# Kernel tuning notes

Hardware: AMD Instinct MI355X
Metric: run time of the kernel (lower is better)

The kernel has to match this reference:

```python
import jax, jax.numpy as jnp
import numpy as np

NUM_HEADS = 8
SIZE_Q = 512
SIZE_K = 512
SIZE_V = 512
B, S = 2, 2048


def setup_inputs() -> dict:
    key = jax.random.key(0)
    ks = jax.random.split(key, 16)
    Hk = SIZE_K  # num_heads * head_size_k
    Hv = SIZE_V  # num_heads * head_size_v
    inp = {
        "k": jax.random.normal(ks[0], (B, S, SIZE_K), jnp.float32),
        "v": jax.random.normal(ks[1], (B, S, SIZE_V), jnp.float32),
        "q": jax.random.normal(ks[2], (B, S, SIZE_Q), jnp.float32),
        "mask": jax.random.randint(ks[3], (S, S), 0, 2).astype(jnp.bool_),
        "spatial_bias": jax.random.normal(ks[4], (1, NUM_HEADS, S, S), jnp.float32),
        # Linear params stored as [in, out]; y = x @ W + b
        "Wq": jax.random.normal(ks[5], (SIZE_Q, Hk), jnp.float32) / np.sqrt(SIZE_Q),
        "bq": jnp.zeros((Hk,), jnp.float32),
        "Wk": jax.random.normal(ks[6], (SIZE_K, Hk), jnp.float32) / np.sqrt(SIZE_K),
        "bk": jnp.zeros((Hk,), jnp.float32),
        "Wv": jax.random.normal(ks[7], (SIZE_V, Hv), jnp.float32) / np.sqrt(SIZE_V),
        "bv": jnp.zeros((Hv,), jnp.float32),
        "Wo": jax.random.normal(ks[8], (Hv, SIZE_V), jnp.float32) / np.sqrt(Hv),
        "bo": jnp.zeros((SIZE_V,), jnp.float32),
    }
    return inp


def reference(k, v, q, mask, spatial_bias, Wq, bq, Wk, bk, Wv, bv, Wo, bo):
    batch, sk = k.shape[0], k.shape[1]
    sq = q.shape[1]
    hdk = Wk.shape[1] // NUM_HEADS
    hdv = Wv.shape[1] // NUM_HEADS
    # QKV projections -> [B, H, S, hd]
    kp = (k @ Wk + bk).reshape(batch, sk, NUM_HEADS, hdk).transpose(0, 2, 1, 3)
    vp = (v @ Wv + bv).reshape(batch, sk, NUM_HEADS, hdv).transpose(0, 2, 1, 3)
    qp = (q @ Wq + bq).reshape(batch, sq, NUM_HEADS, hdk).transpose(0, 2, 1, 3)
    qp = qp / jnp.sqrt(jnp.asarray(hdk, qp.dtype))
    # Scores with additive spatial bias and boolean mask (2D mask -> [1,1,S,S])
    scores = jnp.einsum("bhqd,bhkd->bhqk", qp, kp) + spatial_bias
    scores = jnp.where(mask[None, None, :, :], scores, -jnp.inf)
    attn = jax.nn.softmax(scores, axis=-1)  # dropout=0 (eval)
    ctx = jnp.einsum("bhqk,bhkd->bhqd", attn, vp)
    ctx = ctx.transpose(0, 2, 1, 3).reshape(batch, sq, NUM_HEADS * hdv)
    return ctx @ Wo + bo
```

## Files before the change

kernel.cpp:

```cpp
#include <hip/hip_runtime.h>
#include <hip/hip_bf16.h>

#define S_LEN 2048
#define NH 8
#define HD 64
#define CH 512
#define NEG_BIG (-3.0e38f)
#define SKSPLIT 2
#define KHALF (S_LEN / SKSPLIT)

typedef __bf16 bf16;
typedef bf16 bf16x8 __attribute__((ext_vector_type(8)));
typedef bf16 bf16x4 __attribute__((ext_vector_type(4)));
typedef float floatx4 __attribute__((ext_vector_type(4)));

typedef const unsigned int __attribute__((address_space(1)))* gas1_t;
typedef unsigned int __attribute__((address_space(3)))* las3_t;
__device__ __forceinline__ void gll16(const void* g, void* l) {
    __builtin_amdgcn_global_load_lds((gas1_t)g, (las3_t)l, 16, 0, 0);
}

__global__ void detect_mask_kernel(const unsigned char* __restrict__ mb,
                                   int* __restrict__ flag_out) {
    __shared__ int s1, s3;
    if (threadIdx.x == 0) { s1 = 0; s3 = 0; }
    __syncthreads();
    int any1 = 0, any3 = 0;
    int base = threadIdx.x * 16;
    for (int i = base; i < base + 16; ++i) {
        unsigned char bch = mb[i];
        int m = i & 3;
        if (bch != 0) {
            if (m == 1) any1 = 1;
            if (m == 2 || m == 3) any3 = 1;
        }
    }
    if (any1) atomicOr(&s1, 1);
    if (any3) atomicOr(&s3, 1);
    __syncthreads();
    if (threadIdx.x == 0) {
        int f = 0;
        if (s1) f = 1;
        else if (s3) f = 2;
        *flag_out = f;
    }
}

__global__ __launch_bounds__(256) void prep_weights_kernel(
    const float* __restrict__ Wq, const float* __restrict__ Wk,
    const float* __restrict__ Wv, const float* __restrict__ Wo,
    bf16* __restrict__ WThi, bf16* __restrict__ WTlo)
{
    __shared__ float tile[64][65];
    const int t = threadIdx.x;
    const int n0 = blockIdx.x * 64;
    const int k0 = blockIdx.y * 64;
    const int mat = blockIdx.z;
    const float* W = (mat == 0) ? Wq : (mat == 1) ? Wk : (mat == 2) ? Wv : Wo;
    bf16* hi = WThi + (size_t)mat * (CH * CH);
    bf16* lo = WTlo + (size_t)mat * (CH * CH);
#pragma unroll
    for (int i = 0; i < 4; ++i) {
        int row = (t >> 4) + 16 * i;
        int c4 = (t & 15) << 2;
        float4 f = *(const float4*)(W + (size_t)(k0 + row) * CH + n0 + c4);
        tile[row][c4 + 0] = f.x; tile[row][c4 + 1] = f.y;
        tile[row][c4 + 2] = f.z; tile[row][c4 + 3] = f.w;
    }
    __syncthreads();
#pragma unroll
    for (int i = 0; i < 4; ++i) {
        int nr = (t >> 4) + 16 * i;
        int k4 = (t & 15) << 2;
        bf16x4 h, l;
#pragma unroll
        for (int j = 0; j < 4; ++j) {
            float x = tile[k4 + j][nr];
            bf16 hv = (bf16)x;
            h[j] = hv;
            l[j] = (bf16)(x - (float)hv);
        }
        *(bf16x4*)(hi + (size_t)(n0 + nr) * CH + k0 + k4) = h;
        *(bf16x4*)(lo + (size_t)(n0 + nr) * CH + k0 + k4) = l;
    }
}

__device__ __forceinline__ void gemm_bf16_tile(
    bf16* __restrict__ As_hi, bf16* __restrict__ As_lo,
    bf16* __restrict__ Bs_hi, bf16* __restrict__ Bs_lo,
    const float* __restrict__ IN, const bf16* __restrict__ WThi,
    const bf16* __restrict__ WTlo, const float* __restrict__ BI,
    float* __restrict__ OUT, bf16* __restrict__ OBF, float scale, int mode)
{
    const int t = threadIdx.x;
    const int w = t >> 6;
    const int lane = t & 63;
    const int m16 = lane & 15;
    const int quad = lane >> 4;
    const int m0 = blockIdx.y * 128;
    const int n0 = blockIdx.x * 128;

    const int arow = t >> 1;
    const int akc  = (t & 1) << 4;

    floatx4 acc[2][8];
#pragma unroll
    for (int mi = 0; mi < 2; ++mi)
#pragma unroll
        for (int ni = 0; ni < 8; ++ni) {
            acc[mi][ni][0] = 0.f; acc[mi][ni][1] = 0.f;
            acc[mi][ni][2] = 0.f; acc[mi][ni][3] = 0.f;
        }

    float4 af[4];
    bf16x8 pbh[2], pbl[2];

    auto loadA = [&](int k0) {
        const float* p = IN + (size_t)(m0 + arow) * CH + k0 + akc;
        af[0] = ((const float4*)p)[0];
        af[1] = ((const float4*)p)[1];
        af[2] = ((const float4*)p)[2];
        af[3] = ((const float4*)p)[3];
    };
    auto loadB = [&](int k0) {
        const bf16* ph = WThi + (size_t)(n0 + arow) * CH + k0 + akc;
        const bf16* pl = WTlo + (size_t)(n0 + arow) * CH + k0 + akc;
        pbh[0] = ((const bf16x8*)ph)[0]; pbh[1] = ((const bf16x8*)ph)[1];
        pbl[0] = ((const bf16x8*)pl)[0]; pbl[1] = ((const bf16x8*)pl)[1];
    };
    auto stage = [&]() {
#pragma unroll
        for (int hh = 0; hh < 2; ++hh) {
            bf16x8 h, l;
#pragma unroll
            for (int j = 0; j < 8; ++j) {
                float x = ((const float*)&af[2 * hh])[j];
                bf16 hv = (bf16)x;
                h[j] = hv;
                l[j] = (bf16)(x - (float)hv);
            }
            *(bf16x8*)&As_hi[arow * 40 + akc + 8 * hh] = h;
            *(bf16x8*)&As_lo[arow * 40 + akc + 8 * hh] = l;
        }
        *(bf16x8*)&Bs_hi[arow * 40 + akc + 0] = pbh[0];
        *(bf16x8*)&Bs_hi[arow * 40 + akc + 8] = pbh[1];
        *(bf16x8*)&Bs_lo[arow * 40 + akc + 0] = pbl[0];
        *(bf16x8*)&Bs_lo[arow * 40 + akc + 8] = pbl[1];
    };

    loadA(0); loadB(0);
    for (int ks = 0; ks < CH / 32; ++ks) {
        __syncthreads();
        stage();
        __syncthreads();
        if (ks + 1 < CH / 32) { loadA(32 * (ks + 1)); loadB(32 * (ks + 1)); }

        bf16x8 bh[8], bl[8];
#pragma unroll
        for (int ni = 0; ni < 8; ++ni) {
            bh[ni] = *(const bf16x8*)&Bs_hi[(16 * ni + m16) * 40 + 8 * quad];
            bl[ni] = *(const bf16x8*)&Bs_lo[(16 * ni + m16) * 40 + 8 * quad];
        }
#pragma unroll
        for (int mi = 0; mi < 2; ++mi) {
            bf16x8 ah = *(const bf16x8*)&As_hi[(32 * w + 16 * mi + m16) * 40 + 8 * quad];
            bf16x8 al = *(const bf16x8*)&As_lo[(32 * w + 16 * mi + m16) * 40 + 8 * quad];
#pragma unroll
            for (int ni = 0; ni < 8; ++ni) {
                acc[mi][ni] = __builtin_amdgcn_mfma_f32_16x16x32_bf16(ah, bh[ni], acc[mi][ni], 0, 0, 0);
                acc[mi][ni] = __builtin_amdgcn_mfma_f32_16x16x32_bf16(ah, bl[ni], acc[mi][ni], 0, 0, 0);
                acc[mi][ni] = __builtin_amdgcn_mfma_f32_16x16x32_bf16(al, bh[ni], acc[mi][ni], 0, 0, 0);
            }
        }
    }

#pragma unroll
    for (int mi = 0; mi < 2; ++mi) {
#pragma unroll
        for (int r = 0; r < 4; ++r) {
            int row = m0 + 32 * w + 16 * mi + 4 * quad + r;
            int bb = row >> 11;
            int ss = row & (S_LEN - 1);
#pragma unroll
            for (int ni = 0; ni < 8; ++ni) {
                int col = n0 + 16 * ni + m16;
                float v = (acc[mi][ni][r] + BI[col]) * scale;
                if (mode == 0) {
                    int hh = col >> 6, dd = col & 63;
                    OUT[(((size_t)bb * NH + hh) * S_LEN + ss) * HD + dd] = v;
                } else if (mode == 3) {
                    int hh = col >> 6, dd = col & 63;
                    OBF[((size_t)(bb * NH + hh) * S_LEN + ss) * HD
                        + (((dd >> 3) ^ (ss & 7)) << 3) + (dd & 7)] = (bf16)v;
                } else if (mode == 4) {
                    int hh = col >> 6, dd = col & 63;
                    OBF[((size_t)(bb * NH + hh) * HD + dd) * S_LEN
                        + (ss & ~63) + ((((ss >> 3) & 7) ^ (dd & 7)) << 3) + (ss & 7)] = (bf16)v;
                } else {
                    OUT[(size_t)row * CH + col] = v;
                }
            }
        }
    }
}

__global__ __launch_bounds__(256, 2) void qkv_gemm_kernel(
    const float* __restrict__ q_in, const float* __restrict__ k_in,
    const float* __restrict__ v_in,
    const bf16* __restrict__ WThi, const bf16* __restrict__ WTlo,
    const float* __restrict__ bq, const float* __restrict__ bk,
    const float* __restrict__ bv,
    float* __restrict__ qp, bf16* __restrict__ kswz, bf16* __restrict__ vswz)
{
    __shared__ __attribute__((aligned(16))) bf16 As_hi[128 * 40];
    __shared__ __attribute__((aligned(16))) bf16 As_lo[128 * 40];
    __shared__ __attribute__((aligned(16))) bf16 Bs_hi[128 * 40];
    __shared__ __attribute__((aligned(16))) bf16 Bs_lo[128 * 40];
    int z = blockIdx.z;
    if (z == 0)
        gemm_bf16_tile(As_hi, As_lo, Bs_hi, Bs_lo, q_in,
                       WThi, WTlo, bq, qp, nullptr, 0.125f, 0);
    else if (z == 1)
        gemm_bf16_tile(As_hi, As_lo, Bs_hi, Bs_lo, k_in,
                       WThi + (size_t)CH * CH, WTlo + (size_t)CH * CH, bk,
                       nullptr, kswz, 1.0f, 3);
    else
        gemm_bf16_tile(As_hi, As_lo, Bs_hi, Bs_lo, v_in,
                       WThi + (size_t)2 * CH * CH, WTlo + (size_t)2 * CH * CH, bv,
                       nullptr, vswz, 1.0f, 4);
}

__global__ __launch_bounds__(256, 2) void out_gemm_kernel(
    const float* __restrict__ ctx,
    const bf16* __restrict__ WThi, const bf16* __restrict__ WTlo,
    const float* __restrict__ bo, float* __restrict__ out)
{
    __shared__ __attribute__((aligned(16))) bf16 As_hi[128 * 40];
    __shared__ __attribute__((aligned(16))) bf16 As_lo[128 * 40];
    __shared__ __attribute__((aligned(16))) bf16 Bs_hi[128 * 40];
    __shared__ __attribute__((aligned(16))) bf16 Bs_lo[128 * 40];
    gemm_bf16_tile(As_hi, As_lo, Bs_hi, Bs_lo, ctx,
                   WThi + (size_t)3 * CH * CH, WTlo + (size_t)3 * CH * CH, bo,
                   out, nullptr, 1.0f, 2);
}

__global__ __launch_bounds__(256, 4) void attn_kernel(
    const float* __restrict__ qp, const bf16* __restrict__ kswz,
    const bf16* __restrict__ vswz, const float* __restrict__ bias,
    const void* __restrict__ mask, const int* __restrict__ flagp,
    float* __restrict__ ctxp, float* __restrict__ ml)
{
    __shared__ __attribute__((aligned(16))) bf16 Kt[64 * 64];
    __shared__ __attribute__((aligned(16))) bf16 Vt[64 * 64];
    __shared__ __attribute__((aligned(16))) bf16 Pbf[64 * 72];

    const int t    = threadIdx.x;
    const int w    = t >> 6;
    const int lane = t & 63;
    const int m16  = lane & 15;
    const int quad = lane >> 4;
    const int mx7  = m16 & 7;
    const int q0   = blockIdx.x * 64;
    const int h    = blockIdx.y;
    const int b    = blockIdx.z >> 1;
    const int kz   = blockIdx.z & 1;
    const int bh   = b * NH + h;
    const int flag = *flagp;
    const int kbeg = kz * KHALF;

    bf16x8 qf[2];
    {
        const float* qrow =
            qp + ((size_t)bh * S_LEN + q0 + 16 * w + m16) * HD + 8 * quad;
#pragma unroll
        for (int c = 0; c < 2; ++c) {
            float4 f0 = *(const float4*)(qrow + 32 * c);
            float4 f1 = *(const float4*)(qrow + 32 * c + 4);
            bf16x8 v;
            v[0] = (bf16)f0.x; v[1] = (bf16)f0.y; v[2] = (bf16)f0.z; v[3] = (bf16)f0.w;
            v[4] = (bf16)f1.x; v[5] = (bf16)f1.y; v[6] = (bf16)f1.z; v[7] = (bf16)f1.w;
            qf[c] = v;
        }
    }

    floatx4 ctxa[4];
    float mrow[4], lrow[4];
#pragma unroll
    for (int tt = 0; tt < 4; ++tt) { ctxa[tt][0]=0.f; ctxa[tt][1]=0.f; ctxa[tt][2]=0.f; ctxa[tt][3]=0.f; }
#pragma unroll
    for (int r = 0; r < 4; ++r) { mrow[r] = NEG_BIG; lrow[r] = 0.f; }

    const int qrow0 = q0 + 16 * w + 4 * quad;
    const float* bbase = bias + ((size_t)h * S_LEN + qrow0) * S_LEN + m16;
    const unsigned char* mb8  = (const unsigned char*)mask + (size_t)qrow0 * S_LEN + m16;
    const unsigned int*  mb32 = (const unsigned int*)mask  + (size_t)qrow0 * S_LEN + m16;

    float bnext[16]; unsigned mnext[16]; float mb[16];
    auto prefetchBM = [&](int k0) {
        if (flag == 1) {
#pragma unroll
            for (int r = 0; r < 4; ++r)
#pragma unroll
                for (int tt = 0; tt < 4; ++tt)
                    mnext[4 * r + tt] = mb8[(size_t)r * S_LEN + k0 + 16 * tt];
        } else {
#pragma unroll
            for (int r = 0; r < 4; ++r)
#pragma unroll
                for (int tt = 0; tt < 4; ++tt)
                    mnext[4 * r + tt] = mb32[(size_t)r * S_LEN + k0 + 16 * tt];
        }
#pragma unroll
        for (int r = 0; r < 4; ++r)
#pragma unroll
            for (int tt = 0; tt < 4; ++tt)
                bnext[4 * r + tt] = bbase[(size_t)r * S_LEN + k0 + 16 * tt];
    };
    prefetchBM(kbeg);

    const bf16* kb = kswz + (size_t)bh * S_LEN * HD;
    const bf16* vb = vswz + (size_t)bh * HD * S_LEN;
    const int lrow8 = lane >> 3;
    const int lcol8 = (lane & 7) * 8;

    for (int k0 = kbeg; k0 < kbeg + KHALF; k0 += 64) {
        __syncthreads();
#pragma unroll
        for (int i = 0; i < 2; ++i) {
            int c = 2 * w + i;
            int row = 8 * c + lrow8;
            gll16(kb + (size_t)(k0 + row) * HD + lcol8, &Kt[c * 512]);
            gll16(vb + (size_t)row * S_LEN + k0 + lcol8, &Vt[c * 512]);
        }
        __syncthreads();

#pragma unroll
        for (int j = 0; j < 16; ++j) mb[j] = mnext[j] ? bnext[j] : NEG_BIG;
        if (k0 + 64 < kbeg + KHALF) prefetchBM(k0 + 64);

        floatx4 sc[4];
#pragma unroll
        for (int tt = 0; tt < 4; ++tt) { sc[tt][0]=0.f; sc[tt][1]=0.f; sc[tt][2]=0.f; sc[tt][3]=0.f; }
#pragma unroll
        for (int st = 0; st < 2; ++st)
#pragma unroll
            for (int tt = 0; tt < 4; ++tt) {
                bf16x8 kf = *(const bf16x8*)&Kt[(16 * tt + m16) * 64
                                                + (((quad + 4 * st) ^ mx7) << 3)];
                sc[tt] = __builtin_amdgcn_mfma_f32_16x16x32_bf16(qf[st], kf, sc[tt], 0, 0, 0);
            }

        float alpha[4];
#pragma unroll
        for (int r = 0; r < 4; ++r) {
            int lrowq = 16 * w + 4 * quad + r;
            float s[4];
#pragma unroll
            for (int tt = 0; tt < 4; ++tt)
                s[tt] = sc[tt][r] + mb[4 * r + tt];
            float mx = fmaxf(fmaxf(s[0], s[1]), fmaxf(s[2], s[3]));
            mx = fmaxf(mx, __shfl_xor(mx, 1));
            mx = fmaxf(mx, __shfl_xor(mx, 2));
            mx = fmaxf(mx, __shfl_xor(mx, 4));
            mx = fmaxf(mx, __shfl_xor(mx, 8));
            float mnew = fmaxf(mrow[r], mx);
            float al = __expf(mrow[r] - mnew);
            float ls = 0.f;
#pragma unroll
            for (int tt = 0; tt < 4; ++tt) {
                float p = (s[tt] <= -1e37f) ? 0.f : __expf(s[tt] - mnew);
                ls += p;
                Pbf[lrowq * 72 + 16 * tt + m16] = (bf16)p;
            }
            ls += __shfl_xor(ls, 1);
            ls += __shfl_xor(ls, 2);
            ls += __shfl_xor(ls, 4);
            ls += __shfl_xor(ls, 8);
            lrow[r] = lrow[r] * al + ls;
            mrow[r] = mnew;
            alpha[r] = al;
        }
#pragma unroll
        for (int tt = 0; tt < 4; ++tt)
#pragma unroll
            for (int r = 0; r < 4; ++r) ctxa[tt][r] *= alpha[r];

#pragma unroll
        for (int st = 0; st < 2; ++st) {
            bf16x8 pf = *(const bf16x8*)&Pbf[(16 * w + m16) * 72 + 8 * quad + 32 * st];
#pragma unroll
            for (int tt = 0; tt < 4; ++tt) {
                bf16x8 vf = *(const bf16x8*)&Vt[(16 * tt + m16) * 64
                                                + (((quad + 4 * st) ^ mx7) << 3)];
                ctxa[tt] = __builtin_amdgcn_mfma_f32_16x16x32_bf16(pf, vf, ctxa[tt], 0, 0, 0);
            }
        }
    }

    float* cp = ctxp + (size_t)kz * (2 * NH * S_LEN * HD);
#pragma unroll
    for (int r = 0; r < 4; ++r) {
        int grow = q0 + 16 * w + 4 * quad + r;
        size_t prow = (size_t)bh * S_LEN + grow;
#pragma unroll
        for (int tt = 0; tt < 4; ++tt)
            cp[prow * HD + 16 * tt + m16] = ctxa[tt][r];
        if (m16 == 0) {
            ml[((size_t)kz * (2 * NH * S_LEN) + prow) * 2 + 0] = mrow[r];
            ml[((size_t)kz * (2 * NH * S_LEN) + prow) * 2 + 1] = lrow[r];
        }
    }
}

__global__ __launch_bounds__(256) void merge_kernel(
    const float* __restrict__ ctxp, const float* __restrict__ ml,
    float* __restrict__ ctxo)
{
    const int PHALF = 2 * NH * S_LEN * HD;
    const int MLHALF = 2 * NH * S_LEN;
    int idx = blockIdx.x * 256 + threadIdx.x;
    int d = (idx & 15) << 2;
    int h = (idx >> 4) & (NH - 1);
    int s = (idx >> 7) & (S_LEN - 1);
    int b = idx >> 18;
    size_t prow = ((size_t)b * NH + h) * S_LEN + s;
    float m0 = ml[prow * 2],            l0 = ml[prow * 2 + 1];
    float m1 = ml[(MLHALF + prow) * 2], l1 = ml[(MLHALF + prow) * 2 + 1];
    float mx = fmaxf(m0, m1);
    float a0 = __expf(m0 - mx), a1 = __expf(m1 - mx);
    float den = a0 * l0 + a1 * l1;
    float inv = den > 0.f ? 1.f / den : 0.f;
    float4 c0 = *(const float4*)(ctxp + prow * HD + d);
    float4 c1 = *(const float4*)(ctxp + PHALF + prow * HD + d);
    float4 o;
    o.x = (a0 * c0.x + a1 * c1.x) * inv;
    o.y = (a0 * c0.y + a1 * c1.y) * inv;
    o.z = (a0 * c0.z + a1 * c1.z) * inv;
    o.w = (a0 * c0.w + a1 * c1.w) * inv;
    *(float4*)(ctxo + ((size_t)b * S_LEN + s) * CH + h * HD + d) = o;
}

extern "C" void kernel_launch(void* const* d_in, const int* in_sizes, int n_in,
                              void* d_out, int out_size, void* d_ws, size_t ws_size,
                              hipStream_t stream) {
    const float* k_in = (const float*)d_in[0];
    const float* v_in = (const float*)d_in[1];
    const float* q_in = (const float*)d_in[2];
    const void*  mask = d_in[3];
    const float* bias = (const float*)d_in[4];
    const float* Wq = (const float*)d_in[5];
    const float* bq = (const float*)d_in[6];
    const float* Wk = (const float*)d_in[7];
    const float* bk = (const float*)d_in[8];
    const float* Wv = (const float*)d_in[9];
    const float* bv = (const float*)d_in[10];
    const float* Wo = (const float*)d_in[11];
    const float* bo = (const float*)d_in[12];
    float* out = (float*)d_out;

    char* base = (char*)d_ws;
    float* qp   = (float*)(base);
    float* ctx  = (float*)(base);
    float* ctxp = (float*)(base + (8u  << 20));
    float* mlb  = (float*)(base + (24u << 20));
    bf16*  kswz = (bf16*)(base + (25u << 20));
    bf16*  vswz = (bf16*)(base + (29u << 20));
    bf16*  WThi = (bf16*)(base + (33u << 20));
    bf16*  WTlo = (bf16*)(base + (35u << 20));
    int*   flag = (int*) (base + (37u << 20));

    detect_mask_kernel<<<1, 256, 0, stream>>>((const unsigned char*)mask, flag);
    prep_weights_kernel<<<dim3(8, 8, 4), 256, 0, stream>>>(
        Wq, Wk, Wv, Wo, WThi, WTlo);
    qkv_gemm_kernel<<<dim3(4, 32, 3), 256, 0, stream>>>(
        q_in, k_in, v_in, WThi, WTlo, bq, bk, bv, qp, kswz, vswz);
    attn_kernel<<<dim3(32, 8, 2 * SKSPLIT), 256, 0, stream>>>(
        qp, kswz, vswz, bias, mask, flag, ctxp, mlb);
    merge_kernel<<<2048, 256, 0, stream>>>(ctxp, mlb, ctx);
    out_gemm_kernel<<<dim3(4, 32, 1), 256, 0, stream>>>(
        ctx, WThi, WTlo, bo, out);
}
```

Baseline: 379.6 us.

## Fuse split-K merge into output GEMM, double-buffer K/V, remap attention blocks

Removes the separate merge kernel and instead combines the two split-K partial contexts, using their max and sum statistics, inside the A-tile load of the output projection GEMM. This avoids writing and re-reading an intermediate ctx buffer and saves one kernel launch. The attention kernel now double-buffers the K/V tiles in LDS so the next tile loads while the current one is computed, cutting one barrier per iteration. Block indices are also permuted so that blocks sharing batch, split and head land next to each other, which may improve cache locality. The trade-off is more LDS per block and redundant exp and divide work in each GEMM A load.

```diff
diff --git a/kernel.cpp b/kernel.cpp
--- a/kernel.cpp
+++ b/kernel.cpp
@@ -6,8 +6,9 @@
 #define HD 64
 #define CH 512
 #define NEG_BIG (-3.0e38f)
-#define SKSPLIT 2
-#define KHALF (S_LEN / SKSPLIT)
+#define KHALF 1024
+#define CTXP_STRIDE (2 * NH * S_LEN * HD)
+#define ML_STRIDE   (2 * NH * S_LEN)
 
 typedef __bf16 bf16;
 typedef bf16 bf16x8 __attribute__((ext_vector_type(8)));
@@ -90,7 +91,8 @@
     bf16* __restrict__ Bs_hi, bf16* __restrict__ Bs_lo,
     const float* __restrict__ IN, const bf16* __restrict__ WThi,
     const bf16* __restrict__ WTlo, const float* __restrict__ BI,
-    float* __restrict__ OUT, bf16* __restrict__ OBF, float scale, int mode)
+    float* __restrict__ OUT, bf16* __restrict__ OBF,
+    const float* __restrict__ ML, float scale, int mode)
 {
     const int t = threadIdx.x;
     const int w = t >> 6;
@@ -116,11 +118,37 @@
     bf16x8 pbh[2], pbl[2];
 
     auto loadA = [&](int k0) {
-        const float* p = IN + (size_t)(m0 + arow) * CH + k0 + akc;
-        af[0] = ((const float4*)p)[0];
-        af[1] = ((const float4*)p)[1];
-        af[2] = ((const float4*)p)[2];
-        af[3] = ((const float4*)p)[3];
+        if (ML) {
+            int col = k0 + akc;
+            int hh = col >> 6, dd = col & 63;
+            int row = m0 + arow;
+            int bb = row >> 11, ss = row & (S_LEN - 1);
+            size_t prow = ((size_t)bb * NH + hh) * S_LEN + ss;
+            float m0v = ML[prow * 2],                 l0v = ML[prow * 2 + 1];
+            float m1v = ML[(ML_STRIDE + prow) * 2],   l1v = ML[(ML_STRIDE + prow) * 2 + 1];
+            float mx = fmaxf(m0v, m1v);
+            float e0 = __expf(m0v - mx), e1 = __expf(m1v - mx);
+            float den = e0 * l0v + e1 * l1v;
+            float inv = den > 0.f ? 1.f / den : 0.f;
+            float a0 = e0 * inv, a1 = e1 * inv;
+            const float* p0 = IN + prow * HD + dd;
+            const float* p1 = p0 + CTXP_STRIDE;
+#pragma unroll
+            for (int j = 0; j < 4; ++j) {
+                float4 c0 = ((const float4*)p0)[j];
+                float4 c1 = ((const float4*)p1)[j];
+                af[j].x = a0 * c0.x + a1 * c1.x;
+                af[j].y = a0 * c0.y + a1 * c1.y;
+                af[j].z = a0 * c0.z + a1 * c1.z;
+                af[j].w = a0 * c0.w + a1 * c1.w;
+            }
+        } else {
+            const float* p = IN + (size_t)(m0 + arow) * CH + k0 + akc;
+            af[0] = ((const float4*)p)[0];
+            af[1] = ((const float4*)p)[1];
+            af[2] = ((const float4*)p)[2];
+            af[3] = ((const float4*)p)[3];
+        }
     };
     auto loadB = [&](int k0) {
         const bf16* ph = WThi + (size_t)(n0 + arow) * CH + k0 + akc;
@@ -219,19 +247,19 @@
     int z = blockIdx.z;
     if (z == 0)
         gemm_bf16_tile(As_hi, As_lo, Bs_hi, Bs_lo, q_in,
-                       WThi, WTlo, bq, qp, nullptr, 0.125f, 0);
+                       WThi, WTlo, bq, qp, nullptr, nullptr, 0.125f, 0);
     else if (z == 1)
         gemm_bf16_tile(As_hi, As_lo, Bs_hi, Bs_lo, k_in,
                        WThi + (size_t)CH * CH, WTlo + (size_t)CH * CH, bk,
-                       nullptr, kswz, 1.0f, 3);
+                       nullptr, kswz, nullptr, 1.0f, 3);
     else
         gemm_bf16_tile(As_hi, As_lo, Bs_hi, Bs_lo, v_in,
                        WThi + (size_t)2 * CH * CH, WTlo + (size_t)2 * CH * CH, bv,
-                       nullptr, vswz, 1.0f, 4);
+                       nullptr, vswz, nullptr, 1.0f, 4);
 }
 
 __global__ __launch_bounds__(256, 2) void out_gemm_kernel(
-    const float* __restrict__ ctx,
+    const float* __restrict__ ctxp, const float* __restrict__ ml,
     const bf16* __restrict__ WThi, const bf16* __restrict__ WTlo,
     const float* __restrict__ bo, float* __restrict__ out)
 {
@@ -239,9 +267,9 @@
     __shared__ __attribute__((aligned(16))) bf16 As_lo[128 * 40];
     __shared__ __attribute__((aligned(16))) bf16 Bs_hi[128 * 40];
     __shared__ __attribute__((aligned(16))) bf16 Bs_lo[128 * 40];
-    gemm_bf16_tile(As_hi, As_lo, Bs_hi, Bs_lo, ctx,
+    gemm_bf16_tile(As_hi, As_lo, Bs_hi, Bs_lo, ctxp,
                    WThi + (size_t)3 * CH * CH, WTlo + (size_t)3 * CH * CH, bo,
-                   out, nullptr, 1.0f, 2);
+                   out, nullptr, ml, 1.0f, 2);
 }
 
 __global__ __launch_bounds__(256, 4) void attn_kernel(
@@ -250,8 +278,8 @@
     const void* __restrict__ mask, const int* __restrict__ flagp,
     float* __restrict__ ctxp, float* __restrict__ ml)
 {
-    __shared__ __attribute__((aligned(16))) bf16 Kt[64 * 64];
-    __shared__ __attribute__((aligned(16))) bf16 Vt[64 * 64];
+    __shared__ __attribute__((aligned(16))) bf16 Kt[2][64 * 64];
+    __shared__ __attribute__((aligned(16))) bf16 Vt[2][64 * 64];
     __shared__ __attribute__((aligned(16))) bf16 Pbf[64 * 72];
 
     const int t    = threadIdx.x;
@@ -260,10 +288,15 @@
     const int m16  = lane & 15;
     const int quad = lane >> 4;
     const int mx7  = m16 & 7;
-    const int q0   = blockIdx.x * 64;
-    const int h    = blockIdx.y;
-    const int b    = blockIdx.z >> 1;
-    const int kz   = blockIdx.z & 1;
+
+    const int p  = blockIdx.x + 32 * (blockIdx.y + 8 * blockIdx.z);
+    const int l  = (p & 7) * 128 + (p >> 3);
+    const int b  = l & 1;
+    const int kz = (l >> 1) & 1;
+    const int h  = (l >> 2) & 7;
+    const int qi = l >> 5;
+
+    const int q0   = qi * 64;
     const int bh   = b * NH + h;
     const int flag = *flagp;
     const int kbeg = kz * KHALF;
@@ -316,28 +349,37 @@
             for (int tt = 0; tt < 4; ++tt)
                 bnext[4 * r + tt] = bbase[(size_t)r * S_LEN + k0 + 16 * tt];
     };
-    prefetchBM(kbeg);
 
     const bf16* kb = kswz + (size_t)bh * S_LEN * HD;
     const bf16* vb = vswz + (size_t)bh * HD * S_LEN;
     const int lrow8 = lane >> 3;
     const int lcol8 = (lane & 7) * 8;
 
-    for (int k0 = kbeg; k0 < kbeg + KHALF; k0 += 64) {
-        __syncthreads();
+    auto stageKV = [&](int k0, int buf) {
 #pragma unroll
         for (int i = 0; i < 2; ++i) {
             int c = 2 * w + i;
             int row = 8 * c + lrow8;
-            gll16(kb + (size_t)(k0 + row) * HD + lcol8, &Kt[c * 512]);
-            gll16(vb + (size_t)row * S_LEN + k0 + lcol8, &Vt[c * 512]);
-        }
-        __syncthreads();
+            gll16(kb + (size_t)(k0 + row) * HD + lcol8, &Kt[buf][c * 512]);
+            gll16(vb + (size_t)row * S_LEN + k0 + lcol8, &Vt[buf][c * 512]);
+        }
+    };
+
+    prefetchBM(kbeg);
+    stageKV(kbeg, 0);
+    __syncthreads();
+    int cur = 0;
+
+    for (int k0 = kbeg; k0 < kbeg + KHALF; k0 += 64) {
+        const bool more = (k0 + 64 < kbeg + KHALF);
+        if (more) stageKV(k0 + 64, cur ^ 1);
 
 #pragma unroll
         for (int j = 0; j < 16; ++j) mb[j] = mnext[j] ? bnext[j] : NEG_BIG;
-        if (k0 + 64 < kbeg + KHALF) prefetchBM(k0 + 64);
-
+        if (more) prefetchBM(k0 + 64);
+
+        const bf16* Kc = Kt[cur];
+        const bf16* Vc = Vt[cur];
         floatx4 sc[4];
 #pragma unroll
         for (int tt = 0; tt < 4; ++tt) { sc[tt][0]=0.f; sc[tt][1]=0.f; sc[tt][2]=0.f; sc[tt][3]=0.f; }
@@ -345,7 +387,7 @@
         for (int st = 0; st < 2; ++st)
 #pragma unroll
             for (int tt = 0; tt < 4; ++tt) {
-                bf16x8 kf = *(const bf16x8*)&Kt[(16 * tt + m16) * 64
+                bf16x8 kf = *(const bf16x8*)&Kc[(16 * tt + m16) * 64
                                                 + (((quad + 4 * st) ^ mx7) << 3)];
                 sc[tt] = __builtin_amdgcn_mfma_f32_16x16x32_bf16(qf[st], kf, sc[tt], 0, 0, 0);
             }
@@ -368,9 +410,9 @@
             float ls = 0.f;
 #pragma unroll
             for (int tt = 0; tt < 4; ++tt) {
-                float p = (s[tt] <= -1e37f) ? 0.f : __expf(s[tt] - mnew);
-                ls += p;
-                Pbf[lrowq * 72 + 16 * tt + m16] = (bf16)p;
+                float px = (s[tt] <= -1e37f) ? 0.f : __expf(s[tt] - mnew);
+                ls += px;
+                Pbf[lrowq * 72 + 16 * tt + m16] = (bf16)px;
             }
             ls += __shfl_xor(ls, 1);
             ls += __shfl_xor(ls, 2);
@@ -390,14 +432,17 @@
             bf16x8 pf = *(const bf16x8*)&Pbf[(16 * w + m16) * 72 + 8 * quad + 32 * st];
 #pragma unroll
             for (int tt = 0; tt < 4; ++tt) {
-                bf16x8 vf = *(const bf16x8*)&Vt[(16 * tt + m16) * 64
+                bf16x8 vf = *(const bf16x8*)&Vc[(16 * tt + m16) * 64
                                                 + (((quad + 4 * st) ^ mx7) << 3)];
                 ctxa[tt] = __builtin_amdgcn_mfma_f32_16x16x32_bf16(pf, vf, ctxa[tt], 0, 0, 0);
             }
         }
-    }
-
-    float* cp = ctxp + (size_t)kz * (2 * NH * S_LEN * HD);
+
+        __syncthreads();
+        cur ^= 1;
+    }
+
+    float* cp = ctxp + (size_t)kz * CTXP_STRIDE;
 #pragma unroll
     for (int r = 0; r < 4; ++r) {
         int grow = q0 + 16 * w + 4 * quad + r;
@@ -406,38 +451,10 @@
         for (int tt = 0; tt < 4; ++tt)
             cp[prow * HD + 16 * tt + m16] = ctxa[tt][r];
         if (m16 == 0) {
-            ml[((size_t)kz * (2 * NH * S_LEN) + prow) * 2 + 0] = mrow[r];
-            ml[((size_t)kz * (2 * NH * S_LEN) + prow) * 2 + 1] = lrow[r];
-        }
-    }
-}
-
-__global__ __launch_bounds__(256) void merge_kernel(
-    const float* __restrict__ ctxp, const float* __restrict__ ml,
-    float* __restrict__ ctxo)
-{
-    const int PHALF = 2 * NH * S_LEN * HD;
-    const int MLHALF = 2 * NH * S_LEN;
-    int idx = blockIdx.x * 256 + threadIdx.x;
-    int d = (idx & 15) << 2;
-    int h = (idx >> 4) & (NH - 1);
-    int s = (idx >> 7) & (S_LEN - 1);
-    int b = idx >> 18;
-    size_t prow = ((size_t)b * NH + h) * S_LEN + s;
-    float m0 = ml[prow * 2],            l0 = ml[prow * 2 + 1];
-    float m1 = ml[(MLHALF + prow) * 2], l1 = ml[(MLHALF + prow) * 2 + 1];
-    float mx = fmaxf(m0, m1);
-    float a0 = __expf(m0 - mx), a1 = __expf(m1 - mx);
-    float den = a0 * l0 + a1 * l1;
-    float inv = den > 0.f ? 1.f / den : 0.f;
-    float4 c0 = *(const float4*)(ctxp + prow * HD + d);
-    float4 c1 = *(const float4*)(ctxp + PHALF + prow * HD + d);
-    float4 o;
-    o.x = (a0 * c0.x + a1 * c1.x) * inv;
-    o.y = (a0 * c0.y + a1 * c1.y) * inv;
-    o.z = (a0 * c0.z + a1 * c1.z) * inv;
-    o.w = (a0 * c0.w + a1 * c1.w) * inv;
-    *(float4*)(ctxo + ((size_t)b * S_LEN + s) * CH + h * HD + d) = o;
+            ml[((size_t)kz * ML_STRIDE + prow) * 2 + 0] = mrow[r];
+            ml[((size_t)kz * ML_STRIDE + prow) * 2 + 1] = lrow[r];
+        }
+    }
 }
 
 extern "C" void kernel_launch(void* const* d_in, const int* in_sizes, int n_in,
@@ -460,7 +477,6 @@
 
     char* base = (char*)d_ws;
     float* qp   = (float*)(base);
-    float* ctx  = (float*)(base);
     float* ctxp = (float*)(base + (8u  << 20));
     float* mlb  = (float*)(base + (24u << 20));
     bf16*  kswz = (bf16*)(base + (25u << 20));
@@ -474,9 +490,8 @@
         Wq, Wk, Wv, Wo, WThi, WTlo);
     qkv_gemm_kernel<<<dim3(4, 32, 3), 256, 0, stream>>>(
         q_in, k_in, v_in, WThi, WTlo, bq, bk, bv, qp, kswz, vswz);
-    attn_kernel<<<dim3(32, 8, 2 * SKSPLIT), 256, 0, stream>>>(
+    attn_kernel<<<dim3(32, 8, 4), 256, 0, stream>>>(
         qp, kswz, vswz, bias, mask, flag, ctxp, mlb);
-    merge_kernel<<<2048, 256, 0, stream>>>(ctxp, mlb, ctx);
     out_gemm_kernel<<<dim3(4, 32, 1), 256, 0, stream>>>(
-        ctx, WThi, WTlo, bo, out);
-}
+        ctxp, mlb, WThi, WTlo, bo, out);
+}
```

New measurement: 358.5 us. 5.5% less time.
